# Performance work log

Measured on AMD Instinct MI355X. Metric: run time of the kernel, lower is better.

The kernel has to match this reference:

```python
import jax, jax.numpy as jnp
import numpy as np

NUM_HEADS = 8
NEG_INF = -2**32 + 1  # matches the TF code's masking constant


def setup_inputs() -> dict:
    key = jax.random.key(0)
    ks = jax.random.split(key, 12)
    B, L, D_IN, D_MODEL = 2, 2048, 256, 256
    s = 1.0 / np.sqrt(D_IN)
    return {
        "queries": jax.random.normal(ks[0], (B, L, D_IN), jnp.float32),
        "keys": jax.random.normal(ks[1], (B, L, D_IN), jnp.float32),
        "values": jax.random.normal(ks[2], (B, L, D_IN), jnp.float32),
        "key_mask": jax.random.randint(ks[3], (B, L, 1), 0, 2, jnp.int32),
        "Wq": jax.random.normal(ks[4], (D_IN, D_MODEL), jnp.float32) * s,
        "bq": jnp.zeros((D_MODEL,), jnp.float32),
        "Wk": jax.random.normal(ks[5], (D_IN, D_MODEL), jnp.float32) * s,
        "bk": jnp.zeros((D_MODEL,), jnp.float32),
        "Wv": jax.random.normal(ks[6], (D_IN, D_MODEL), jnp.float32) * s,
        "bv": jnp.zeros((D_MODEL,), jnp.float32),
        "Wo": jax.random.normal(ks[7], (D_MODEL, D_IN), jnp.float32) * s,
        "bo": jnp.zeros((D_IN,), jnp.float32),
    }


def reference(queries, keys, values, key_mask, Wq, bq, Wk, bk, Wv, bv, Wo, bo):
    B, Lq, _ = queries.shape
    Lk = keys.shape[1]
    h = NUM_HEADS
    d_model = Wq.shape[1]
    depth = d_model // h

    Q = queries @ Wq + bq  # [B, Lq, d_model]
    K = keys @ Wk + bk     # [B, Lk, d_model]
    V = values @ Wv + bv   # [B, Lk, d_model]

    # split heads: contiguous chunks of size depth along feature dim
    Qh = Q.reshape(B, Lq, h, depth)
    Kh = K.reshape(B, Lk, h, depth)
    Vh = V.reshape(B, Lk, h, depth)

    scores = jnp.einsum("bqhd,bkhd->bhqk", Qh, Kh) / jnp.sqrt(
        jnp.asarray(depth, jnp.float32)
    )  # [B, h, Lq, Lk]

    # key_mask: [B, Lk, 1] -> broadcast over heads and query positions
    mask = (key_mask[:, None, :, 0] != 0)[:, :, None, :]  # [B, 1, 1, Lk]
    scores = jnp.where(mask, scores, jnp.asarray(NEG_INF, scores.dtype))

    attn = jax.nn.softmax(scores, axis=-1)  # dropout is identity at inference
    out = jnp.einsum("bhqk,bkhd->bqhd", attn, Vh).reshape(B, Lq, d_model)
    return out @ Wo + bo  # [B, Lq, input_dim]
```

## Files before the change

### kernel.cpp

```cpp
#include <hip/hip_runtime.h>

#define Bn 2
#define Ln 2048
#define DIN 256
#define Hn 8
#define DEPTH 32
#define SCALE 0.17677669529663687f
#define NEGC (-4294967296.0f)

typedef _Float16 f16;
typedef _Float16 h8 __attribute__((ext_vector_type(8)));
typedef _Float16 h4 __attribute__((ext_vector_type(4)));
typedef float f4 __attribute__((ext_vector_type(4)));

#define WLS 264
#define NG  (Ln / 16)


__global__ __launch_bounds__(256) void proj_gemm(
    const float* __restrict__ Xq, const float* __restrict__ Xk, const float* __restrict__ Xv,
    const float* __restrict__ Wq, const float* __restrict__ Wk, const float* __restrict__ Wv,
    const float* __restrict__ bq, const float* __restrict__ bk, const float* __restrict__ bv,
    f16* __restrict__ Qz, f16* __restrict__ Kz, f16* __restrict__ Vz)
{
    __shared__ f16 Wl[64 * WLS];
    const int p = blockIdx.z;
    const float* X = p == 0 ? Xq : p == 1 ? Xk : Xv;
    const float* W = p == 0 ? Wq : p == 1 ? Wk : Wv;
    const float* bias = p == 0 ? bq : p == 1 ? bk : bv;

    const int t = threadIdx.x, w = t >> 6, lane = t & 63;
    const int l15 = lane & 15, quad = lane >> 4;
    const int n0 = blockIdx.y * 64;

    {
        const int nl = t & 63, kb = t >> 6;
        for (int kk = 0; kk < 64; ++kk) {
            const int k = kk * 4 + kb;
            Wl[nl * WLS + k] = (f16)W[(size_t)k * DIN + n0 + nl];
        }
    }
    __syncthreads();

    const int m0w = blockIdx.x * 128 + w * 32;
    const float* A0 = X + (size_t)(m0w + l15) * DIN;
    const float* A1 = X + (size_t)(m0w + 16 + l15) * DIN;

    f4 acc[2][4];
    #pragma unroll
    for (int mi = 0; mi < 2; ++mi)
        #pragma unroll
        for (int tt = 0; tt < 4; ++tt) acc[mi][tt] = (f4){0.f, 0.f, 0.f, 0.f};

    for (int k0 = 0; k0 < DIN; k0 += 32) {
        float4 xa0 = *(const float4*)(A0 + k0 + quad * 8);
        float4 xb0 = *(const float4*)(A0 + k0 + quad * 8 + 4);
        float4 xa1 = *(const float4*)(A1 + k0 + quad * 8);
        float4 xb1 = *(const float4*)(A1 + k0 + quad * 8 + 4);
        h8 af0 = { (f16)xa0.x, (f16)xa0.y, (f16)xa0.z, (f16)xa0.w,
                   (f16)xb0.x, (f16)xb0.y, (f16)xb0.z, (f16)xb0.w };
        h8 af1 = { (f16)xa1.x, (f16)xa1.y, (f16)xa1.z, (f16)xa1.w,
                   (f16)xb1.x, (f16)xb1.y, (f16)xb1.z, (f16)xb1.w };
        #pragma unroll
        for (int tt = 0; tt < 4; ++tt) {
            h8 bf = *(const h8*)(Wl + (tt * 16 + l15) * WLS + k0 + quad * 8);
            acc[0][tt] = __builtin_amdgcn_mfma_f32_16x16x32_f16(af0, bf, acc[0][tt], 0, 0, 0);
            acc[1][tt] = __builtin_amdgcn_mfma_f32_16x16x32_f16(af1, bf, acc[1][tt], 0, 0, 0);
        }
    }
    #pragma unroll
    for (int mi = 0; mi < 2; ++mi)
        #pragma unroll
        for (int tt = 0; tt < 4; ++tt) {
            const int c = n0 + tt * 16 + l15;
            const float bb = bias[c];
            const int h = c >> 5, dd = c & 31;
            #pragma unroll
            for (int r = 0; r < 4; ++r) {
                const int row = m0w + mi * 16 + quad * 4 + r;
                const int b = row >> 11, l = row & (Ln - 1);
                const float v = acc[mi][tt][r] + bb;
                const size_t hbg = (size_t)(b * Hn + h) * NG + (l >> 4);
                if (p == 0)
                    Qz[(hbg * 64 + (dd >> 3) * 16 + (l & 15)) * 8 + (dd & 7)] =
                        (f16)(v * SCALE);
                else if (p == 1)
                    Kz[(hbg * 64 + (dd >> 3) * 16 + (l & 15)) * 8 + (dd & 7)] = (f16)v;
                else
                    Vz[((hbg * 2 + (dd >> 4)) * 64 + ((l & 15) >> 2) * 16 + (dd & 15)) * 4
                       + (l & 3)] = (f16)v;
            }
        }
}

__global__ __launch_bounds__(256) void flash_mfma(
    const f16* __restrict__ Qz, const f16* __restrict__ Kz,
    const f16* __restrict__ Vz, const int* __restrict__ mask,
    f16* __restrict__ Oz)
{
    __shared__ float Os[4][32][68];
    __shared__ float lS[4][64];
    const int t = threadIdx.x, w = t >> 6, lane = t & 63;
    const int l15 = lane & 15, quad = lane >> 4;
    const int hb = blockIdx.x;
    const int q0 = blockIdx.y * 64;
    const int b = hb >> 3, h = hb & 7;
    const f16* Qh = Qz + (size_t)hb * NG * 512;
    const f16* Kh = Kz + (size_t)hb * NG * 512;
    const f16* Vh = Vz + (size_t)hb * NG * 512;
    const int* mrow = mask + b * Ln;
    const int k_base = w * (Ln / 4);

    h8 qf[4];
    #pragma unroll
    for (int qg = 0; qg < 4; ++qg)
        qf[qg] = *(const h8*)(Qh + ((size_t)(q0 / 16 + qg) * 64 + lane) * 8);

    f4 o[2][4];
    #pragma unroll
    for (int i = 0; i < 2; ++i)
        #pragma unroll
        for (int j = 0; j < 4; ++j) o[i][j] = (f4){0.f, 0.f, 0.f, 0.f};
    float l_run[4] = {0.f, 0.f, 0.f, 0.f};

    for (int kt = 0; kt < Ln / 4 / 64; ++kt) {
        const int k0 = k_base + kt * 64;
        #pragma unroll
        for (int tt = 0; tt < 4; ++tt) {
            const int g = (k0 >> 4) + tt;
            h8 kf = *(const h8*)(Kh + ((size_t)g * 64 + lane) * 8);
            const int4 mk = *(const int4*)(mrow + g * 16 + quad * 4);
            f4 bias4 = { mk.x ? 0.f : NEGC, mk.y ? 0.f : NEGC,
                         mk.z ? 0.f : NEGC, mk.w ? 0.f : NEGC };
            h4 va0 = *(const h4*)(Vh + ((size_t)(g * 2)     * 64 + lane) * 4);
            h4 va1 = *(const h4*)(Vh + ((size_t)(g * 2 + 1) * 64 + lane) * 4);
            f4 s[4];
            #pragma unroll
            for (int qg = 0; qg < 4; ++qg)
                s[qg] = __builtin_amdgcn_mfma_f32_16x16x32_f16(kf, qf[qg], bias4, 0, 0, 0);
            #pragma unroll
            for (int qg = 0; qg < 4; ++qg) {
                h4 pf;
                #pragma unroll
                for (int r = 0; r < 4; ++r) {
                    const float pv = __expf(s[qg][r]);
                    l_run[qg] += pv;
                    pf[r] = (f16)pv;
                }
                o[0][qg] = __builtin_amdgcn_mfma_f32_16x16x16f16(va0, pf, o[0][qg], 0, 0, 0);
                o[1][qg] = __builtin_amdgcn_mfma_f32_16x16x16f16(va1, pf, o[1][qg], 0, 0, 0);
            }
        }
    }
    #pragma unroll
    for (int qg = 0; qg < 4; ++qg) {
        l_run[qg] += __shfl_xor(l_run[qg], 16, 64);
        l_run[qg] += __shfl_xor(l_run[qg], 32, 64);
        if (quad == 0) lS[w][qg * 16 + l15] = l_run[qg];
        #pragma unroll
        for (int dg = 0; dg < 2; ++dg)
            #pragma unroll
            for (int r = 0; r < 4; ++r)
                Os[w][dg * 16 + quad * 4 + r][qg * 16 + l15] = o[dg][qg][r];
    }
    __syncthreads();

    {
        const int cq = t & 63, dv = t >> 6;
        const float ls = lS[0][cq] + lS[1][cq] + lS[2][cq] + lS[3][cq];
        const float inv = 1.0f / ls;
        h8 pack;
        #pragma unroll
        for (int i = 0; i < 8; ++i) {
            const int dd = dv * 8 + i;
            const float ov = Os[0][dd][cq] + Os[1][dd][cq] +
                             Os[2][dd][cq] + Os[3][dd][cq];
            pack[i] = (f16)(ov * inv);
        }
        const int gm = b * NG + ((q0 + cq) >> 4);
        *(h8*)(Oz + (((size_t)gm * 8 + h) * 64 + dv * 16 + (cq & 15)) * 8) = pack;
    }
}

__global__ __launch_bounds__(256) void out_gemm(
    const f16* __restrict__ Oz, const float* __restrict__ Wo,
    const float* __restrict__ bo, float* __restrict__ out)
{
    __shared__ f16 Wl[64 * WLS];
    const int t = threadIdx.x, w = t >> 6, lane = t & 63;
    const int l15 = lane & 15, quad = lane >> 4;
    const int m0 = blockIdx.x * 64 + w * 16;
    const int n0 = blockIdx.y * 64;

    {
        const int nl = t & 63, kb = t >> 6;
        for (int kk = 0; kk < 64; ++kk) {
            const int k = kk * 4 + kb;
            Wl[nl * WLS + k] = (f16)Wo[(size_t)k * DIN + n0 + nl];
        }
    }
    __syncthreads();

    const int gm = m0 >> 4;

    f4 acc[4] = {{0.f,0.f,0.f,0.f},{0.f,0.f,0.f,0.f},{0.f,0.f,0.f,0.f},{0.f,0.f,0.f,0.f}};
    for (int k0 = 0; k0 < DIN; k0 += 32) {
        const int h = k0 >> 5;
        h8 af = *(const h8*)(Oz + (((size_t)gm * 8 + h) * 64 + lane) * 8);
        #pragma unroll
        for (int tt = 0; tt < 4; ++tt) {
            h8 bf = *(const h8*)(Wl + (tt * 16 + l15) * WLS + k0 + quad * 8);
            acc[tt] = __builtin_amdgcn_mfma_f32_16x16x32_f16(af, bf, acc[tt], 0, 0, 0);
        }
    }
    #pragma unroll
    for (int tt = 0; tt < 4; ++tt) {
        const int c = n0 + tt * 16 + l15;
        const float bb = bo[c];
        #pragma unroll
        for (int r = 0; r < 4; ++r)
            out[(size_t)(m0 + quad * 4 + r) * DIN + c] = acc[tt][r] + bb;
    }
}

#define QT 128
#define KT 32
#define TS 34
#define SST (KT + 1)

__global__ __launch_bounds__(512) void fb_fused_attn(
    const float* __restrict__ Xq, const float* __restrict__ Xk,
    const float* __restrict__ Xv, const int* __restrict__ mask,
    const float* __restrict__ Wq, const float* __restrict__ bq,
    const float* __restrict__ Wk, const float* __restrict__ bk,
    const float* __restrict__ Wv, const float* __restrict__ bv,
    float* __restrict__ out)
{
    __shared__ float Qs[QT * TS];
    __shared__ float Ks[KT * TS];
    __shared__ float Vs[KT * TS];
    __shared__ float Ss[QT * SST];
    __shared__ float mrow[QT], lrow[QT], arow[QT];
    __shared__ int mk[KT];

    const int t = threadIdx.x;
    const int d = t & 31;
    const int rg = t >> 5;
    const int q0 = blockIdx.x * QT;
    const int h = blockIdx.y;
    const int b = blockIdx.z;
    const int hc = h * DEPTH + d;

    {
        const float bqv = bq[hc];
        for (int i = 0; i < 8; ++i) {
            const int r = rg + 16 * i;
            const float* x = Xq + ((size_t)(b * Ln + q0 + r)) * DIN;
            float acc = bqv;
            #pragma unroll 8
            for (int k = 0; k < DIN; ++k) acc = fmaf(x[k], Wq[k * DIN + hc], acc);
            Qs[r * TS + d] = acc * SCALE;
        }
    }
    if (t < QT) { mrow[t] = -INFINITY; lrow[t] = 0.f; }
    float o_acc[8];
    #pragma unroll
    for (int i = 0; i < 8; ++i) o_acc[i] = 0.f;

    const float bkv = bk[hc], bvv = bv[hc];

    for (int kt = 0; kt < Ln / KT; ++kt) {
        const int k0 = kt * KT;
        #pragma unroll
        for (int i = 0; i < 2; ++i) {
            const int r = rg + 16 * i;
            const float* xk = Xk + ((size_t)(b * Ln + k0 + r)) * DIN;
            const float* xv = Xv + ((size_t)(b * Ln + k0 + r)) * DIN;
            float aK = bkv, aV = bvv;
            #pragma unroll 4
            for (int k = 0; k < DIN; ++k) {
                aK = fmaf(xk[k], Wk[k * DIN + hc], aK);
                aV = fmaf(xv[k], Wv[k * DIN + hc], aV);
            }
            Ks[r * TS + d] = aK;
            Vs[r * TS + d] = aV;
        }
        if (t < KT) mk[t] = mask[b * Ln + k0 + t];
        __syncthreads();

        for (int idx = t; idx < QT * KT; idx += 512) {
            const int r = idx >> 5, k = idx & (KT - 1);
            const float2* qv = (const float2*)(Qs + r * TS);
            const float2* kv = (const float2*)(Ks + k * TS);
            float s = 0.f;
            #pragma unroll
            for (int j = 0; j < 16; ++j) {
                float2 a = qv[j], c = kv[j];
                s += a.x * c.x + a.y * c.y;
            }
            Ss[r * SST + k] = mk[k] ? s : NEGC;
        }
        __syncthreads();

        if (t < QT) {
            float tm = -INFINITY;
            #pragma unroll 8
            for (int k = 0; k < KT; ++k) tm = fmaxf(tm, Ss[t * SST + k]);
            const float nm = fmaxf(mrow[t], tm);
            arow[t] = __expf(mrow[t] - nm);
            mrow[t] = nm;
        }
        __syncthreads();

        for (int idx = t; idx < QT * KT; idx += 512) {
            const int r = idx >> 5, k = idx & (KT - 1);
            Ss[r * SST + k] = __expf(Ss[r * SST + k] - mrow[r]);
        }
        __syncthreads();

        if (t < QT) {
            float rs = 0.f;
            #pragma unroll 8
            for (int k = 0; k < KT; ++k) rs += Ss[t * SST + k];
            lrow[t] = arow[t] * lrow[t] + rs;
        }
        #pragma unroll
        for (int i = 0; i < 8; ++i) {
            const int r = rg + 16 * i;
            const float a = arow[r];
            float acc = o_acc[i] * a;
            const float* pr = Ss + r * SST;
            const float* vc = Vs + d;
            #pragma unroll 8
            for (int k = 0; k < KT; ++k) acc = fmaf(pr[k], vc[k * TS], acc);
            o_acc[i] = acc;
        }
        __syncthreads();
    }
    #pragma unroll
    for (int i = 0; i < 8; ++i) {
        const int r = rg + 16 * i;
        out[((size_t)(b * Ln + q0 + r)) * DIN + hc] = o_acc[i] / lrow[r];
    }
}

__global__ __launch_bounds__(256) void fb_out_proj(
    const float* __restrict__ Wo, const float* __restrict__ bo,
    float* __restrict__ out)
{
    __shared__ float xr[4][DIN];
    const int col = threadIdx.x;
    const int r0 = blockIdx.x * 4;
    #pragma unroll
    for (int rr = 0; rr < 4; ++rr)
        xr[rr][col] = out[(size_t)(r0 + rr) * DIN + col];
    __syncthreads();
    const float bb = bo[col];
    float a0 = bb, a1 = bb, a2 = bb, a3 = bb;
    #pragma unroll 4
    for (int k = 0; k < DIN; ++k) {
        const float w = Wo[k * DIN + col];
        a0 = fmaf(xr[0][k], w, a0);
        a1 = fmaf(xr[1][k], w, a1);
        a2 = fmaf(xr[2][k], w, a2);
        a3 = fmaf(xr[3][k], w, a3);
    }
    float* o = out + (size_t)r0 * DIN + col;
    o[0] = a0; o[DIN] = a1; o[2 * DIN] = a2; o[3 * DIN] = a3;
}

extern "C" void kernel_launch(void* const* d_in, const int* in_sizes, int n_in,
                              void* d_out, int out_size, void* d_ws, size_t ws_size,
                              hipStream_t stream) {
    const float* Xq = (const float*)d_in[0];
    const float* Xk = (const float*)d_in[1];
    const float* Xv = (const float*)d_in[2];
    const int* mask = (const int*)d_in[3];
    const float* Wq = (const float*)d_in[4];
    const float* bq = (const float*)d_in[5];
    const float* Wk = (const float*)d_in[6];
    const float* bk = (const float*)d_in[7];
    const float* Wv = (const float*)d_in[8];
    const float* bv = (const float*)d_in[9];
    const float* Wo = (const float*)d_in[10];
    const float* bo = (const float*)d_in[11];
    float* out = (float*)d_out;

    const size_t HB_E = (size_t)Bn * Hn * Ln * DEPTH;
    const size_t need = 4 * HB_E * sizeof(f16);

    if (ws_size >= need) {
        f16* Qz = (f16*)d_ws;
        f16* Kz = Qz + HB_E;
        f16* Vz = Kz + HB_E;
        f16* Oz = Vz + HB_E;
        proj_gemm<<<dim3(Bn * Ln / 128, DIN / 64, 3), 256, 0, stream>>>(
            Xq, Xk, Xv, Wq, Wk, Wv, bq, bk, bv, Qz, Kz, Vz);
        flash_mfma<<<dim3(Bn * Hn, Ln / 64), 256, 0, stream>>>(Qz, Kz, Vz, mask, Oz);
        out_gemm<<<dim3(Bn * Ln / 64, DIN / 64), 256, 0, stream>>>(Oz, Wo, bo, out);
    } else {
        fb_fused_attn<<<dim3(Ln / QT, Hn, Bn), 512, 0, stream>>>(
            Xq, Xk, Xv, mask, Wq, bq, Wk, bk, Wv, bv, out);
        fb_out_proj<<<Bn * Ln / 4, 256, 0, stream>>>(Wo, bo, out);
    }
}
```

Before: 125.0 us.

## Fuse Q projection, attention and output projection into one persistent kernel with grid barriers

The three-kernel pipeline becomes two kernels. K/V projections are written into the output buffer, used as scratch, with K and V interleaved per tile. A single 512-block kernel computes its Q tile directly with MFMA, runs flash attention, then uses two software grid barriers to stage the attention output in the same buffer and apply the output projection. This removes launch overhead and the Q/O workspace round trips. In exchange it relies on all 512 blocks being co-resident for the spin barrier and reads Wq/Wo straight from global memory with scalar loads.

```diff
diff --git a/kernel.cpp b/kernel.cpp
--- a/kernel.cpp
+++ b/kernel.cpp
@@ -7,27 +7,44 @@
 #define DEPTH 32
 #define SCALE 0.17677669529663687f
 #define NEGC (-4294967296.0f)
+#define NG  (Ln / 16)
+#define WLS 264
+#define NBLK 512
 
 typedef _Float16 f16;
 typedef _Float16 h8 __attribute__((ext_vector_type(8)));
 typedef _Float16 h4 __attribute__((ext_vector_type(4)));
 typedef float f4 __attribute__((ext_vector_type(4)));
 
-#define WLS 264
-#define NG  (Ln / 16)
-
-
-__global__ __launch_bounds__(256) void proj_gemm(
-    const float* __restrict__ Xq, const float* __restrict__ Xk, const float* __restrict__ Xv,
-    const float* __restrict__ Wq, const float* __restrict__ Wk, const float* __restrict__ Wv,
-    const float* __restrict__ bq, const float* __restrict__ bk, const float* __restrict__ bv,
-    f16* __restrict__ Qz, f16* __restrict__ Kz, f16* __restrict__ Vz)
+
+__device__ int g_bar = 0;
+
+__device__ __forceinline__ void grid_bar() {
+    __threadfence();
+    __syncthreads();
+    if (threadIdx.x == 0) {
+        int tk = __hip_atomic_fetch_add(&g_bar, 1, __ATOMIC_ACQ_REL,
+                                        __HIP_MEMORY_SCOPE_AGENT) + 1;
+        int target = ((tk + NBLK - 1) / NBLK) * NBLK;
+        while (__hip_atomic_load(&g_bar, __ATOMIC_ACQUIRE,
+                                 __HIP_MEMORY_SCOPE_AGENT) < target)
+            __builtin_amdgcn_s_sleep(8);
+    }
+    __syncthreads();
+    __threadfence();
+}
+
+__global__ __launch_bounds__(256) void proj_kv(
+    const float* __restrict__ Xk, const float* __restrict__ Xv,
+    const float* __restrict__ Wk, const float* __restrict__ Wv,
+    const float* __restrict__ bk, const float* __restrict__ bv,
+    f16* __restrict__ S)
 {
     __shared__ f16 Wl[64 * WLS];
     const int p = blockIdx.z;
-    const float* X = p == 0 ? Xq : p == 1 ? Xk : Xv;
-    const float* W = p == 0 ? Wq : p == 1 ? Wk : Wv;
-    const float* bias = p == 0 ? bq : p == 1 ? bk : bv;
+    const float* X = p ? Xv : Xk;
+    const float* W = p ? Wv : Wk;
+    const float* bias = p ? bv : bk;
 
     const int t = threadIdx.x, w = t >> 6, lane = t & 63;
     const int l15 = lane & 15, quad = lane >> 4;
@@ -81,40 +98,77 @@
                 const int b = row >> 11, l = row & (Ln - 1);
                 const float v = acc[mi][tt][r] + bb;
                 const size_t hbg = (size_t)(b * Hn + h) * NG + (l >> 4);
-                if (p == 0)
-                    Qz[(hbg * 64 + (dd >> 3) * 16 + (l & 15)) * 8 + (dd & 7)] =
-                        (f16)(v * SCALE);
-                else if (p == 1)
-                    Kz[(hbg * 64 + (dd >> 3) * 16 + (l & 15)) * 8 + (dd & 7)] = (f16)v;
-                else
-                    Vz[((hbg * 2 + (dd >> 4)) * 64 + ((l & 15) >> 2) * 16 + (dd & 15)) * 4
-                       + (l & 3)] = (f16)v;
-            }
-        }
-}
-
-__global__ __launch_bounds__(256) void flash_mfma(
-    const f16* __restrict__ Qz, const f16* __restrict__ Kz,
-    const f16* __restrict__ Vz, const int* __restrict__ mask,
-    f16* __restrict__ Oz)
+                if (!p) {
+                    const size_t i = (hbg * 64 + (size_t)(dd >> 3) * 16 + (l & 15)) * 8 + (dd & 7);
+                    S[(i >> 8) * 512 + 256 + (i & 255)] = (f16)v;
+                } else {
+                    const size_t i = ((hbg * 2 + (dd >> 4)) * 64 + (size_t)((l & 15) >> 2) * 16
+                                      + (dd & 15)) * 4 + (l & 3);
+                    S[(i >> 8) * 512 + (i & 255)] = (f16)v;
+                }
+            }
+        }
+}
+
+__global__ __launch_bounds__(256, 2) void fused_attn_out(
+    const float* __restrict__ Xq, const float* __restrict__ Wq,
+    const float* __restrict__ bq, const int* __restrict__ mask,
+    const float* __restrict__ Wo, const float* __restrict__ bo,
+    float* out)
 {
-    __shared__ float Os[4][32][68];
-    __shared__ float lS[4][64];
+    __shared__ union {
+        f16 Qs[4 * 512];
+        struct { float Os[4][32][68]; float lS[4][64]; } c;
+    } sm;
+
+    f16* S = (f16*)out;
     const int t = threadIdx.x, w = t >> 6, lane = t & 63;
     const int l15 = lane & 15, quad = lane >> 4;
-    const int hb = blockIdx.x;
-    const int q0 = blockIdx.y * 64;
-    const int b = hb >> 3, h = hb & 7;
-    const f16* Qh = Qz + (size_t)hb * NG * 512;
-    const f16* Kh = Kz + (size_t)hb * NG * 512;
-    const f16* Vh = Vz + (size_t)hb * NG * 512;
+    const int hb = blockIdx.x >> 5, qc = blockIdx.x & 31;
+    const int b = hb >> 3, h = hb & 7, q0 = qc * 64;
+
+    {
+        const float* A0 = Xq + (size_t)(b * Ln + q0 + w * 16 + l15) * DIN;
+        const float* Wp = Wq + h * 32 + l15;
+        f4 a2[2] = { {0.f,0.f,0.f,0.f}, {0.f,0.f,0.f,0.f} };
+        #pragma unroll
+        for (int kk = 0; kk < 8; ++kk) {
+            const int k0 = kk * 32;
+            float4 xa = *(const float4*)(A0 + k0 + quad * 8);
+            float4 xb = *(const float4*)(A0 + k0 + quad * 8 + 4);
+            h8 af = { (f16)xa.x, (f16)xa.y, (f16)xa.z, (f16)xa.w,
+                      (f16)xb.x, (f16)xb.y, (f16)xb.z, (f16)xb.w };
+            #pragma unroll
+            for (int tt = 0; tt < 2; ++tt) {
+                h8 bf;
+                #pragma unroll
+                for (int j = 0; j < 8; ++j)
+                    bf[j] = (f16)Wp[(size_t)(k0 + quad * 8 + j) * DIN + tt * 16];
+                a2[tt] = __builtin_amdgcn_mfma_f32_16x16x32_f16(af, bf, a2[tt], 0, 0, 0);
+            }
+        }
+        #pragma unroll
+        for (int tt = 0; tt < 2; ++tt) {
+            const int c = tt * 16 + l15;
+            const float bb = bq[h * 32 + c];
+            #pragma unroll
+            for (int r = 0; r < 4; ++r) {
+                const int lc = quad * 4 + r;
+                sm.Qs[((size_t)w * 64 + (c >> 3) * 16 + lc) * 8 + (c & 7)] =
+                    (f16)((a2[tt][r] + bb) * SCALE);
+            }
+        }
+    }
+    __syncthreads();
+    h8 qf[4];
+    #pragma unroll
+    for (int qg = 0; qg < 4; ++qg)
+        qf[qg] = *(const h8*)(sm.Qs + ((size_t)qg * 64 + lane) * 8);
+    __syncthreads();
+
     const int* mrow = mask + b * Ln;
-    const int k_base = w * (Ln / 4);
-
-    h8 qf[4];
-    #pragma unroll
-    for (int qg = 0; qg < 4; ++qg)
-        qf[qg] = *(const h8*)(Qh + ((size_t)(q0 / 16 + qg) * 64 + lane) * 8);
+    const f16* Kb = S + (size_t)hb * NG * 1024 + 256 + (lane >> 5) * 512 + (lane & 31) * 8;
+    const f16* Vb = S + (size_t)hb * NG * 1024 + lane * 4;
 
     f4 o[2][4];
     #pragma unroll
@@ -122,28 +176,29 @@
         #pragma unroll
         for (int j = 0; j < 4; ++j) o[i][j] = (f4){0.f, 0.f, 0.f, 0.f};
     float l_run[4] = {0.f, 0.f, 0.f, 0.f};
+    const int k_base = w * (Ln / 4);
 
     for (int kt = 0; kt < Ln / 4 / 64; ++kt) {
         const int k0 = k_base + kt * 64;
         #pragma unroll
         for (int tt = 0; tt < 4; ++tt) {
             const int g = (k0 >> 4) + tt;
-            h8 kf = *(const h8*)(Kh + ((size_t)g * 64 + lane) * 8);
+            h8 kf = *(const h8*)(Kb + (size_t)g * 1024);
             const int4 mk = *(const int4*)(mrow + g * 16 + quad * 4);
             f4 bias4 = { mk.x ? 0.f : NEGC, mk.y ? 0.f : NEGC,
                          mk.z ? 0.f : NEGC, mk.w ? 0.f : NEGC };
-            h4 va0 = *(const h4*)(Vh + ((size_t)(g * 2)     * 64 + lane) * 4);
-            h4 va1 = *(const h4*)(Vh + ((size_t)(g * 2 + 1) * 64 + lane) * 4);
-            f4 s[4];
+            h4 va0 = *(const h4*)(Vb + (size_t)g * 1024);
+            h4 va1 = *(const h4*)(Vb + (size_t)g * 1024 + 512);
+            f4 s_[4];
             #pragma unroll
             for (int qg = 0; qg < 4; ++qg)
-                s[qg] = __builtin_amdgcn_mfma_f32_16x16x32_f16(kf, qf[qg], bias4, 0, 0, 0);
+                s_[qg] = __builtin_amdgcn_mfma_f32_16x16x32_f16(kf, qf[qg], bias4, 0, 0, 0);
             #pragma unroll
             for (int qg = 0; qg < 4; ++qg) {
                 h4 pf;
                 #pragma unroll
                 for (int r = 0; r < 4; ++r) {
-                    const float pv = __expf(s[qg][r]);
+                    const float pv = __expf(s_[qg][r]);
                     l_run[qg] += pv;
                     pf[r] = (f16)pv;
                 }
@@ -156,226 +211,74 @@
     for (int qg = 0; qg < 4; ++qg) {
         l_run[qg] += __shfl_xor(l_run[qg], 16, 64);
         l_run[qg] += __shfl_xor(l_run[qg], 32, 64);
-        if (quad == 0) lS[w][qg * 16 + l15] = l_run[qg];
+        if (quad == 0) sm.c.lS[w][qg * 16 + l15] = l_run[qg];
         #pragma unroll
         for (int dg = 0; dg < 2; ++dg)
             #pragma unroll
             for (int r = 0; r < 4; ++r)
-                Os[w][dg * 16 + quad * 4 + r][qg * 16 + l15] = o[dg][qg][r];
-    }
-    __syncthreads();
-
-    {
-        const int cq = t & 63, dv = t >> 6;
-        const float ls = lS[0][cq] + lS[1][cq] + lS[2][cq] + lS[3][cq];
-        const float inv = 1.0f / ls;
-        h8 pack;
-        #pragma unroll
-        for (int i = 0; i < 8; ++i) {
-            const int dd = dv * 8 + i;
-            const float ov = Os[0][dd][cq] + Os[1][dd][cq] +
-                             Os[2][dd][cq] + Os[3][dd][cq];
-            pack[i] = (f16)(ov * inv);
-        }
-        const int gm = b * NG + ((q0 + cq) >> 4);
-        *(h8*)(Oz + (((size_t)gm * 8 + h) * 64 + dv * 16 + (cq & 15)) * 8) = pack;
-    }
-}
-
-__global__ __launch_bounds__(256) void out_gemm(
-    const f16* __restrict__ Oz, const float* __restrict__ Wo,
-    const float* __restrict__ bo, float* __restrict__ out)
-{
-    __shared__ f16 Wl[64 * WLS];
-    const int t = threadIdx.x, w = t >> 6, lane = t & 63;
-    const int l15 = lane & 15, quad = lane >> 4;
-    const int m0 = blockIdx.x * 64 + w * 16;
-    const int n0 = blockIdx.y * 64;
-
-    {
-        const int nl = t & 63, kb = t >> 6;
-        for (int kk = 0; kk < 64; ++kk) {
-            const int k = kk * 4 + kb;
-            Wl[nl * WLS + k] = (f16)Wo[(size_t)k * DIN + n0 + nl];
-        }
-    }
-    __syncthreads();
-
-    const int gm = m0 >> 4;
-
-    f4 acc[4] = {{0.f,0.f,0.f,0.f},{0.f,0.f,0.f,0.f},{0.f,0.f,0.f,0.f},{0.f,0.f,0.f,0.f}};
-    for (int k0 = 0; k0 < DIN; k0 += 32) {
-        const int h = k0 >> 5;
-        h8 af = *(const h8*)(Oz + (((size_t)gm * 8 + h) * 64 + lane) * 8);
-        #pragma unroll
-        for (int tt = 0; tt < 4; ++tt) {
-            h8 bf = *(const h8*)(Wl + (tt * 16 + l15) * WLS + k0 + quad * 8);
-            acc[tt] = __builtin_amdgcn_mfma_f32_16x16x32_f16(af, bf, acc[tt], 0, 0, 0);
-        }
-    }
-    #pragma unroll
-    for (int tt = 0; tt < 4; ++tt) {
-        const int c = n0 + tt * 16 + l15;
-        const float bb = bo[c];
-        #pragma unroll
-        for (int r = 0; r < 4; ++r)
-            out[(size_t)(m0 + quad * 4 + r) * DIN + c] = acc[tt][r] + bb;
-    }
-}
-
-#define QT 128
-#define KT 32
-#define TS 34
-#define SST (KT + 1)
-
-__global__ __launch_bounds__(512) void fb_fused_attn(
-    const float* __restrict__ Xq, const float* __restrict__ Xk,
-    const float* __restrict__ Xv, const int* __restrict__ mask,
-    const float* __restrict__ Wq, const float* __restrict__ bq,
-    const float* __restrict__ Wk, const float* __restrict__ bk,
-    const float* __restrict__ Wv, const float* __restrict__ bv,
-    float* __restrict__ out)
-{
-    __shared__ float Qs[QT * TS];
-    __shared__ float Ks[KT * TS];
-    __shared__ float Vs[KT * TS];
-    __shared__ float Ss[QT * SST];
-    __shared__ float mrow[QT], lrow[QT], arow[QT];
-    __shared__ int mk[KT];
-
-    const int t = threadIdx.x;
-    const int d = t & 31;
-    const int rg = t >> 5;
-    const int q0 = blockIdx.x * QT;
-    const int h = blockIdx.y;
-    const int b = blockIdx.z;
-    const int hc = h * DEPTH + d;
-
-    {
-        const float bqv = bq[hc];
-        for (int i = 0; i < 8; ++i) {
-            const int r = rg + 16 * i;
-            const float* x = Xq + ((size_t)(b * Ln + q0 + r)) * DIN;
-            float acc = bqv;
-            #pragma unroll 8
-            for (int k = 0; k < DIN; ++k) acc = fmaf(x[k], Wq[k * DIN + hc], acc);
-            Qs[r * TS + d] = acc * SCALE;
-        }
-    }
-    if (t < QT) { mrow[t] = -INFINITY; lrow[t] = 0.f; }
-    float o_acc[8];
-    #pragma unroll
-    for (int i = 0; i < 8; ++i) o_acc[i] = 0.f;
-
-    const float bkv = bk[hc], bvv = bv[hc];
-
-    for (int kt = 0; kt < Ln / KT; ++kt) {
-        const int k0 = kt * KT;
-        #pragma unroll
-        for (int i = 0; i < 2; ++i) {
-            const int r = rg + 16 * i;
-            const float* xk = Xk + ((size_t)(b * Ln + k0 + r)) * DIN;
-            const float* xv = Xv + ((size_t)(b * Ln + k0 + r)) * DIN;
-            float aK = bkv, aV = bvv;
-            #pragma unroll 4
-            for (int k = 0; k < DIN; ++k) {
-                aK = fmaf(xk[k], Wk[k * DIN + hc], aK);
-                aV = fmaf(xv[k], Wv[k * DIN + hc], aV);
-            }
-            Ks[r * TS + d] = aK;
-            Vs[r * TS + d] = aV;
-        }
-        if (t < KT) mk[t] = mask[b * Ln + k0 + t];
+                sm.c.Os[w][dg * 16 + quad * 4 + r][qg * 16 + l15] = o[dg][qg][r];
+    }
+    __syncthreads();
+
+    const int cq = t & 63, dv = t >> 6;
+    const float ls = sm.c.lS[0][cq] + sm.c.lS[1][cq] + sm.c.lS[2][cq] + sm.c.lS[3][cq];
+    const float inv = 1.0f / ls;
+    h8 pack;
+    #pragma unroll
+    for (int i = 0; i < 8; ++i) {
+        const int dd = dv * 8 + i;
+        const float ov = sm.c.Os[0][dd][cq] + sm.c.Os[1][dd][cq] +
+                         sm.c.Os[2][dd][cq] + sm.c.Os[3][dd][cq];
+        pack[i] = (f16)(ov * inv);
+    }
+
+    grid_bar();
+
+    *(h8*)(S + (size_t)(b * Ln + q0 + cq) * 512 + h * 32 + dv * 8) = pack;
+
+    grid_bar();
+
+    if (blockIdx.x < 256) {
+        const int m0 = blockIdx.x * 16;
+        h8 af[8];
+        #pragma unroll
+        for (int kk = 0; kk < 8; ++kk)
+            af[kk] = *(const h8*)(S + (size_t)(m0 + l15) * 512 + kk * 32 + quad * 8);
         __syncthreads();
 
-        for (int idx = t; idx < QT * KT; idx += 512) {
-            const int r = idx >> 5, k = idx & (KT - 1);
-            const float2* qv = (const float2*)(Qs + r * TS);
-            const float2* kv = (const float2*)(Ks + k * TS);
-            float s = 0.f;
-            #pragma unroll
-            for (int j = 0; j < 16; ++j) {
-                float2 a = qv[j], c = kv[j];
-                s += a.x * c.x + a.y * c.y;
-            }
-            Ss[r * SST + k] = mk[k] ? s : NEGC;
-        }
-        __syncthreads();
-
-        if (t < QT) {
-            float tm = -INFINITY;
-            #pragma unroll 8
-            for (int k = 0; k < KT; ++k) tm = fmaxf(tm, Ss[t * SST + k]);
-            const float nm = fmaxf(mrow[t], tm);
-            arow[t] = __expf(mrow[t] - nm);
-            mrow[t] = nm;
-        }
-        __syncthreads();
-
-        for (int idx = t; idx < QT * KT; idx += 512) {
-            const int r = idx >> 5, k = idx & (KT - 1);
-            Ss[r * SST + k] = __expf(Ss[r * SST + k] - mrow[r]);
-        }
-        __syncthreads();
-
-        if (t < QT) {
-            float rs = 0.f;
-            #pragma unroll 8
-            for (int k = 0; k < KT; ++k) rs += Ss[t * SST + k];
-            lrow[t] = arow[t] * lrow[t] + rs;
-        }
-        #pragma unroll
-        for (int i = 0; i < 8; ++i) {
-            const int r = rg + 16 * i;
-            const float a = arow[r];
-            float acc = o_acc[i] * a;
-            const float* pr = Ss + r * SST;
-            const float* vc = Vs + d;
-            #pragma unroll 8
-            for (int k = 0; k < KT; ++k) acc = fmaf(pr[k], vc[k * TS], acc);
-            o_acc[i] = acc;
-        }
-        __syncthreads();
-    }
-    #pragma unroll
-    for (int i = 0; i < 8; ++i) {
-        const int r = rg + 16 * i;
-        out[((size_t)(b * Ln + q0 + r)) * DIN + hc] = o_acc[i] / lrow[r];
-    }
-}
-
-__global__ __launch_bounds__(256) void fb_out_proj(
-    const float* __restrict__ Wo, const float* __restrict__ bo,
-    float* __restrict__ out)
-{
-    __shared__ float xr[4][DIN];
-    const int col = threadIdx.x;
-    const int r0 = blockIdx.x * 4;
-    #pragma unroll
-    for (int rr = 0; rr < 4; ++rr)
-        xr[rr][col] = out[(size_t)(r0 + rr) * DIN + col];
-    __syncthreads();
-    const float bb = bo[col];
-    float a0 = bb, a1 = bb, a2 = bb, a3 = bb;
-    #pragma unroll 4
-    for (int k = 0; k < DIN; ++k) {
-        const float w = Wo[k * DIN + col];
-        a0 = fmaf(xr[0][k], w, a0);
-        a1 = fmaf(xr[1][k], w, a1);
-        a2 = fmaf(xr[2][k], w, a2);
-        a3 = fmaf(xr[3][k], w, a3);
-    }
-    float* o = out + (size_t)r0 * DIN + col;
-    o[0] = a0; o[DIN] = a1; o[2 * DIN] = a2; o[3 * DIN] = a3;
+        const float* Wop = Wo + w * 64 + l15;
+        f4 a4[4];
+        #pragma unroll
+        for (int tt = 0; tt < 4; ++tt) a4[tt] = (f4){0.f, 0.f, 0.f, 0.f};
+        #pragma unroll
+        for (int tt = 0; tt < 4; ++tt)
+            #pragma unroll
+            for (int kk = 0; kk < 8; ++kk) {
+                h8 bf;
+                #pragma unroll
+                for (int j = 0; j < 8; ++j)
+                    bf[j] = (f16)Wop[(size_t)(kk * 32 + quad * 8 + j) * DIN + tt * 16];
+                a4[tt] = __builtin_amdgcn_mfma_f32_16x16x32_f16(af[kk], bf, a4[tt], 0, 0, 0);
+            }
+        #pragma unroll
+        for (int tt = 0; tt < 4; ++tt) {
+            const int c = w * 64 + tt * 16 + l15;
+            const float bb = bo[c];
+            #pragma unroll
+            for (int r = 0; r < 4; ++r)
+                out[(size_t)(m0 + quad * 4 + r) * DIN + c] = a4[tt][r] + bb;
+        }
+    }
 }
 
 extern "C" void kernel_launch(void* const* d_in, const int* in_sizes, int n_in,
                               void* d_out, int out_size, void* d_ws, size_t ws_size,
                               hipStream_t stream) {
+    (void)in_sizes; (void)n_in; (void)d_ws; (void)ws_size; (void)out_size;
     const float* Xq = (const float*)d_in[0];
     const float* Xk = (const float*)d_in[1];
     const float* Xv = (const float*)d_in[2];
-    const int* mask = (const int*)d_in[3];
+    const int*  mask = (const int*)d_in[3];
     const float* Wq = (const float*)d_in[4];
     const float* bq = (const float*)d_in[5];
     const float* Wk = (const float*)d_in[6];
@@ -386,21 +289,8 @@
     const float* bo = (const float*)d_in[11];
     float* out = (float*)d_out;
 
-    const size_t HB_E = (size_t)Bn * Hn * Ln * DEPTH;
-    const size_t need = 4 * HB_E * sizeof(f16);
-
-    if (ws_size >= need) {
-        f16* Qz = (f16*)d_ws;
-        f16* Kz = Qz + HB_E;
-        f16* Vz = Kz + HB_E;
-        f16* Oz = Vz + HB_E;
-        proj_gemm<<<dim3(Bn * Ln / 128, DIN / 64, 3), 256, 0, stream>>>(
-            Xq, Xk, Xv, Wq, Wk, Wv, bq, bk, bv, Qz, Kz, Vz);
-        flash_mfma<<<dim3(Bn * Hn, Ln / 64), 256, 0, stream>>>(Qz, Kz, Vz, mask, Oz);
-        out_gemm<<<dim3(Bn * Ln / 64, DIN / 64), 256, 0, stream>>>(Oz, Wo, bo, out);
-    } else {
-        fb_fused_attn<<<dim3(Ln / QT, Hn, Bn), 512, 0, stream>>>(
-            Xq, Xk, Xv, mask, Wq, bq, Wk, bk, Wv, bv, out);
-        fb_out_proj<<<Bn * Ln / 4, 256, 0, stream>>>(Wo, bo, out);
-    }
-}
+    proj_kv<<<dim3(Bn * Ln / 128, DIN / 64, 2), 256, 0, stream>>>(
+        Xk, Xv, Wk, Wv, bk, bv, (f16*)out);
+    fused_attn_out<<<dim3(NBLK), 256, 0, stream>>>(
+        Xq, Wq, bq, mask, Wo, bo, out);
+}
```

Result: slower. 361.4 us (+189.1%).
